# Optimization experiments

Hardware: AMD Instinct MI355X
Metric: run time of the kernel (lower is better)

## Reference

```python
import jax, jax.numpy as jnp
import numpy as np

THRESHOLD_FACTOR = 1.25


def setup_inputs() -> dict:
    key = jax.random.key(0)
    B, S, D = 2, 4096, 2
    r_embed = jax.random.normal(key, (B, S, D), dtype=jnp.float32)
    return {"r_embed": r_embed}


def reference(r_embed) -> jnp.ndarray:
    # r_embed: [B, S, 2]
    B, S, _ = r_embed.shape
    diff = r_embed[:, :, None, :] - r_embed[:, None, :, :]   # [B, S, S, 2]
    dx, dy = diff[..., 0], diff[..., 1]
    dist_sq = dx * dx + dy * dy                               # [B, S, S]
    # Safe atan2: at (0,0) (diagonal) atan2 returns 0 either way; the where
    # only guards against NaN gradients, forward value is identical.
    zero_pair = (dx == 0) & (dy == 0)
    phase_diff = jnp.arctan2(jnp.where(zero_pair, 0.0, dy),
                             jnp.where(zero_pair, 1.0, dx))
    forward_bias = 0.5 * (1.0 + jnp.cos(phase_diff))          # [B, S, S]
    mean_dist = jnp.mean(dist_sq, axis=(-1, -2), keepdims=True)
    # torch.std defaults to unbiased (ddof=1)
    std_dist = jnp.std(dist_sq, axis=(-1, -2), keepdims=True, ddof=1)
    threshold = mean_dist + THRESHOLD_FACTOR * std_dist
    causal_mask = jnp.tril(jnp.ones((S, S), dtype=bool))      # [S, S]
    valid_mask = (dist_sq <= threshold) & causal_mask[None]
    attention = valid_mask.astype(r_embed.dtype) * forward_bias
    return attention
```

## Files before the change

kernel.cpp:

```cpp
#include <hip/hip_runtime.h>
#include <math.h>

__global__ __launch_bounds__(1024) void pab_moments_kernel(
        const float* __restrict__ r, float* __restrict__ thr_out, int S) {
    const int b = blockIdx.x;
    const float2* emb = (const float2*)r + (size_t)b * S;
    const int tid = threadIdx.x;

    double s[12];
#pragma unroll
    for (int k = 0; k < 12; ++k) s[k] = 0.0;

    for (int idx0 = tid * 4; idx0 < S; idx0 += blockDim.x * 4) {
        float4 c0 = *(const float4*)(emb + idx0);
        float4 c1 = *(const float4*)(emb + idx0 + 2);
        float xs[4] = {c0.x, c0.z, c1.x, c1.z};
        float ys[4] = {c0.y, c0.w, c1.y, c1.w};
#pragma unroll
        for (int k = 0; k < 4; ++k) {
            if (idx0 + k >= S) break;
            double x = (double)xs[k], y = (double)ys[k];
            double x2 = x * x, y2 = y * y;
            s[0]  += x;        s[1]  += y;
            s[2]  += x2;       s[3]  += y2;
            s[4]  += x2 * x;   s[5]  += y2 * y;
            s[6]  += x2 * x2;  s[7]  += y2 * y2;
            s[8]  += x * y;    s[9]  += x2 * y;
            s[10] += x * y2;   s[11] += x2 * y2;
        }
    }

#pragma unroll
    for (int off = 32; off > 0; off >>= 1) {
#pragma unroll
        for (int k = 0; k < 12; ++k)
            s[k] += __shfl_down(s[k], off, 64);
    }

    __shared__ double part[16][12];
    __shared__ double tot[12];
    const int wave = tid >> 6, lane = tid & 63;
    const int nwaves = blockDim.x >> 6;
    if (lane == 0) {
#pragma unroll
        for (int k = 0; k < 12; ++k) part[wave][k] = s[k];
    }
    __syncthreads();
    if (tid < 12) {
        double t = 0.0;
        for (int w = 0; w < nwaves; ++w) t += part[w][tid];
        tot[tid] = t;
    }
    __syncthreads();

    if (tid == 0) {
        double N = (double)S;
        double M = N * N;
        double S1x = tot[0], S1y = tot[1], S2x = tot[2], S2y = tot[3];
        double S3x = tot[4], S3y = tot[5], S4x = tot[6], S4y = tot[7];
        double A11 = tot[8], A21 = tot[9], A12 = tot[10], A22 = tot[11];

        double sum_d = 2.0 * N * (S2x + S2y) - 2.0 * (S1x * S1x + S1y * S1y);
        double qx = 2.0 * N * S4x - 8.0 * S3x * S1x + 6.0 * S2x * S2x;
        double qy = 2.0 * N * S4y - 8.0 * S3y * S1y + 6.0 * S2y * S2y;
        double cross = 2.0 * N * A22 - 4.0 * A21 * S1y - 4.0 * A12 * S1x
                     + 2.0 * S2x * S2y + 4.0 * A11 * A11;
        double sum_d2 = qx + qy + 2.0 * cross;

        double mean = sum_d / M;
        double var  = (sum_d2 - sum_d * sum_d / M) / (M - 1.0);
        thr_out[b] = (float)(mean + 1.25 * sqrt(var));
    }
}

#define PAB_ROWS 16

__global__ __launch_bounds__(256) void pab_attn_kernel(
        const float* __restrict__ r, const float* __restrict__ thr_ws,
        float* __restrict__ out, int S) {
    const int b = blockIdx.z;
    const int i0 = blockIdx.y * PAB_ROWS;
    const int j0 = (blockIdx.x * blockDim.x + threadIdx.x) * 4;
    if (j0 >= S) return;

    const float2* emb = (const float2*)r + (size_t)b * S;
    const float thr = thr_ws[b];

    float4 c0 = *(const float4*)(emb + j0);
    float4 c1 = *(const float4*)(emb + j0 + 2);
    const float xs[4] = {c0.x, c0.z, c1.x, c1.z};
    const float ys[4] = {c0.y, c0.w, c1.y, c1.w};

    size_t orow = ((size_t)b * S + i0) * S + j0;
#pragma unroll
    for (int rr = 0; rr < PAB_ROWS; ++rr) {
        const int i = i0 + rr;
        if (i >= S) break;
        const float2 pi = emb[i];
        float4 res;
        float* rp = &res.x;
#pragma unroll
        for (int k = 0; k < 4; ++k) {
            float dx = pi.x - xs[k];
            float dy = pi.y - ys[k];
            float d2 = fmaf(dx, dx, dy * dy);
            float bias = (d2 > 0.0f) ? fmaf(0.5f * dx, rsqrtf(d2), 0.5f) : 1.0f;
            bool valid = (d2 <= thr) & ((j0 + k) <= i);
            rp[k] = valid ? bias : 0.0f;
        }
        *(float4*)(out + orow) = res;
        orow += S;
    }
}

extern "C" void kernel_launch(void* const* d_in, const int* in_sizes, int n_in,
                              void* d_out, int out_size, void* d_ws, size_t ws_size,
                              hipStream_t stream) {
    const float* r = (const float*)d_in[0];
    float* out = (float*)d_out;
    float* thr = (float*)d_ws;

    long in0 = in_sizes[0];
    int S = (int)((2L * (long)out_size) / in0);
    int B = (int)(in0 / (2L * S));

    pab_moments_kernel<<<dim3(B), dim3(1024), 0, stream>>>(r, thr, S);

    dim3 block(256);
    dim3 grid((S + 1023) / 1024, (S + PAB_ROWS - 1) / PAB_ROWS, B);
    pab_attn_kernel<<<grid, block, 0, stream>>>(r, thr, out, S);
}
```

Before: 144.4 us.

## Fuse threshold moments into attention kernel and fast-path fully masked tiles

Merges the moment-reduction kernel into the attention kernel so every block recomputes the per-batch threshold in double precision from all S points, removing the second launch and its workspace round trip. Blocks lying entirely above the diagonal now write zeros without doing any math, and the row embeddings are preloaded into registers. The cost is that every block repeats an S-length double-precision reduction (2048 blocks, each with 4 loads and dozens of FP64 ops per thread), which may outweigh the launch saving since the kernel is write-bound.

```diff
diff --git a/kernel.cpp b/kernel.cpp
--- a/kernel.cpp
+++ b/kernel.cpp
@@ -1,9 +1,12 @@
 #include <hip/hip_runtime.h>
 #include <math.h>
 
-__global__ __launch_bounds__(1024) void pab_moments_kernel(
-        const float* __restrict__ r, float* __restrict__ thr_out, int S) {
-    const int b = blockIdx.x;
+#define PAB_ROWS 16
+#define PAB_TPB  256
+
+__global__ __launch_bounds__(PAB_TPB) void pab_fused_kernel(
+        const float* __restrict__ r, float* __restrict__ out, int S) {
+    const int b = blockIdx.z;
     const float2* emb = (const float2*)r + (size_t)b * S;
     const int tid = threadIdx.x;
 
@@ -11,7 +14,7 @@
 #pragma unroll
     for (int k = 0; k < 12; ++k) s[k] = 0.0;
 
-    for (int idx0 = tid * 4; idx0 < S; idx0 += blockDim.x * 4) {
+    for (int idx0 = tid * 4; idx0 < S; idx0 += PAB_TPB * 4) {
         float4 c0 = *(const float4*)(emb + idx0);
         float4 c1 = *(const float4*)(emb + idx0 + 2);
         float xs[4] = {c0.x, c0.z, c1.x, c1.z};
@@ -37,10 +40,10 @@
             s[k] += __shfl_down(s[k], off, 64);
     }
 
-    __shared__ double part[16][12];
+    __shared__ double part[PAB_TPB / 64][12];
     __shared__ double tot[12];
+    __shared__ float thr_sh;
     const int wave = tid >> 6, lane = tid & 63;
-    const int nwaves = blockDim.x >> 6;
     if (lane == 0) {
 #pragma unroll
         for (int k = 0; k < 12; ++k) part[wave][k] = s[k];
@@ -48,11 +51,11 @@
     __syncthreads();
     if (tid < 12) {
         double t = 0.0;
-        for (int w = 0; w < nwaves; ++w) t += part[w][tid];
+#pragma unroll
+        for (int w = 0; w < PAB_TPB / 64; ++w) t += part[w][tid];
         tot[tid] = t;
     }
     __syncthreads();
-
     if (tid == 0) {
         double N = (double)S;
         double M = N * N;
@@ -69,46 +72,57 @@
 
         double mean = sum_d / M;
         double var  = (sum_d2 - sum_d * sum_d / M) / (M - 1.0);
-        thr_out[b] = (float)(mean + 1.25 * sqrt(var));
+        thr_sh = (float)(mean + 1.25 * sqrt(var));
     }
-}
+    __syncthreads();
+    const float thr = thr_sh;
 
-#define PAB_ROWS 16
-
-__global__ __launch_bounds__(256) void pab_attn_kernel(
-        const float* __restrict__ r, const float* __restrict__ thr_ws,
-        float* __restrict__ out, int S) {
-    const int b = blockIdx.z;
     const int i0 = blockIdx.y * PAB_ROWS;
-    const int j0 = (blockIdx.x * blockDim.x + threadIdx.x) * 4;
+    const int jt0 = blockIdx.x * PAB_TPB * 4;
+    const int j0 = jt0 + tid * 4;
     if (j0 >= S) return;
 
-    const float2* emb = (const float2*)r + (size_t)b * S;
-    const float thr = thr_ws[b];
+    size_t orow = ((size_t)b * S + i0) * S + j0;
+
+    if (jt0 > i0 + PAB_ROWS - 1) {
+        const float4 z = {0.0f, 0.0f, 0.0f, 0.0f};
+#pragma unroll
+        for (int rr = 0; rr < PAB_ROWS; ++rr) {
+            if (i0 + rr < S) *(float4*)(out + orow) = z;
+            orow += S;
+        }
+        return;
+    }
+
+    float2 pis[PAB_ROWS];
+#pragma unroll
+    for (int rr = 0; rr < PAB_ROWS; ++rr)
+        pis[rr] = emb[min(i0 + rr, S - 1)];
 
     float4 c0 = *(const float4*)(emb + j0);
     float4 c1 = *(const float4*)(emb + j0 + 2);
     const float xs[4] = {c0.x, c0.z, c1.x, c1.z};
     const float ys[4] = {c0.y, c0.w, c1.y, c1.w};
 
-    size_t orow = ((size_t)b * S + i0) * S + j0;
 #pragma unroll
     for (int rr = 0; rr < PAB_ROWS; ++rr) {
         const int i = i0 + rr;
-        if (i >= S) break;
-        const float2 pi = emb[i];
-        float4 res;
-        float* rp = &res.x;
+        if (i < S) {
+            const float2 pi = pis[rr];
+            float4 res;
+            float* rp = &res.x;
 #pragma unroll
-        for (int k = 0; k < 4; ++k) {
-            float dx = pi.x - xs[k];
-            float dy = pi.y - ys[k];
-            float d2 = fmaf(dx, dx, dy * dy);
-            float bias = (d2 > 0.0f) ? fmaf(0.5f * dx, rsqrtf(d2), 0.5f) : 1.0f;
-            bool valid = (d2 <= thr) & ((j0 + k) <= i);
-            rp[k] = valid ? bias : 0.0f;
+            for (int k = 0; k < 4; ++k) {
+                float dx = pi.x - xs[k];
+                float dy = pi.y - ys[k];
+                float d2 = fmaf(dx, dx, dy * dy);
+                float bias = (d2 > 0.0f) ? fmaf(0.5f * dx, rsqrtf(d2), 0.5f)
+                                         : 1.0f;
+                bool valid = (d2 <= thr) & ((j0 + k) <= i);
+                rp[k] = valid ? bias : 0.0f;
+            }
+            *(float4*)(out + orow) = res;
         }
-        *(float4*)(out + orow) = res;
         orow += S;
     }
 }
@@ -118,15 +132,14 @@
                               hipStream_t stream) {
     const float* r = (const float*)d_in[0];
     float* out = (float*)d_out;
-    float* thr = (float*)d_ws;
+    (void)d_ws; (void)ws_size;
 
     long in0 = in_sizes[0];
     int S = (int)((2L * (long)out_size) / in0);
     int B = (int)(in0 / (2L * S));
 
-    pab_moments_kernel<<<dim3(B), dim3(1024), 0, stream>>>(r, thr, S);
-
-    dim3 block(256);
-    dim3 grid((S + 1023) / 1024, (S + PAB_ROWS - 1) / PAB_ROWS, B);
-    pab_attn_kernel<<<grid, block, 0, stream>>>(r, thr, out, S);
+    dim3 block(PAB_TPB);
+    dim3 grid((S + PAB_TPB * 4 - 1) / (PAB_TPB * 4),
+              (S + PAB_ROWS - 1) / PAB_ROWS, B);
+    pab_fused_kernel<<<grid, block, 0, stream>>>(r, out, S);
 }
```

Result: faster. 141.4 us (-2.1%).
